# Kernel optimization log

Measured on AMD Instinct MI355X. Metric: run time of the kernel, lower is better.

The kernel has to match this reference:

```python
import jax, jax.numpy as jnp
import numpy as np

HID = 3584
NH = 16
NKV = 8
HD = 256
T = 2048
THETA = 10000.0
SCALE = 256.0 ** -0.5          # query_pre_attn_scalar ** -0.5
SOFT_CAP = 50.0                # Gemma2 attn_logits_soft_cap


def setup_inputs() -> dict:
    key = jax.random.key(0)
    k1, k2, k3 = jax.random.split(key, 3)
    return {
        "positions": jnp.arange(T, dtype=jnp.int32),
        "hidden_states": jax.random.normal(k1, (T, HID), dtype=jnp.float32),
        "w_qkv": jax.random.normal(k2, (HID, (NH + 2 * NKV) * HD), dtype=jnp.float32) * 0.02,
        "w_o": jax.random.normal(k3, (NH * HD, HID), dtype=jnp.float32) * 0.02,
    }


def _apply_rope(x, positions):
    # neox-style rotary embedding over full head_dim
    d = x.shape[-1]
    inv_freq = 1.0 / (THETA ** (jnp.arange(0, d, 2, dtype=jnp.float32) / d))  # [d/2]
    freqs = positions.astype(jnp.float32)[:, None] * inv_freq[None, :]        # [T, d/2]
    cos = jnp.concatenate([jnp.cos(freqs)] * 2, axis=-1)[:, None, :]          # [T,1,d]
    sin = jnp.concatenate([jnp.sin(freqs)] * 2, axis=-1)[:, None, :]
    x1, x2 = jnp.split(x, 2, axis=-1)
    rotated = jnp.concatenate([-x2, x1], axis=-1)
    return x * cos + rotated * sin


def reference(positions, hidden_states, w_qkv, w_o):
    t = hidden_states.shape[0]
    qkv = hidden_states @ w_qkv                                   # [T, (NH+2*NKV)*HD]
    q = qkv[:, : NH * HD].reshape(t, NH, HD)
    k = qkv[:, NH * HD:(NH + NKV) * HD].reshape(t, NKV, HD)
    v = qkv[:, (NH + NKV) * HD:].reshape(t, NKV, HD)

    q = _apply_rope(q, positions)
    k = _apply_rope(k, positions)

    rep = NH // NKV                                               # GQA expansion
    k = jnp.repeat(k, rep, axis=1)                                # [T, NH, HD]
    v = jnp.repeat(v, rep, axis=1)

    scores = jnp.einsum("qhd,khd->hqk", q, k) * SCALE             # [NH, T, T]
    scores = SOFT_CAP * jnp.tanh(scores / SOFT_CAP)               # logit soft-cap
    causal = jnp.tril(jnp.ones((t, t), dtype=bool))
    scores = jnp.where(causal[None, :, :], scores, -jnp.inf)
    probs = jax.nn.softmax(scores, axis=-1)
    out = jnp.einsum("hqk,khd->qhd", probs, v).reshape(t, NH * HD)
    return out @ w_o                                              # [T, HID]
```

## Files before the change

kernel.cpp:

```cpp
#include <hip/hip_runtime.h>
#include <hip/hip_bf16.h>


#define T_SEQ 2048
#define HID_DIM 3584
#define NH 16
#define NKV 8
#define HD 256
#define QKV_N ((NH + 2 * NKV) * HD)
#define ATT_N (NH * HD)
#define V_OFF ((NH + NKV) * HD)

typedef __bf16 bf16_t;
typedef bf16_t bf16x8 __attribute__((ext_vector_type(8)));
typedef float f32x4 __attribute__((ext_vector_type(4)));

__device__ __forceinline__ void gload16(const bf16_t* g, bf16_t* l) {
  __builtin_amdgcn_global_load_lds(
      (const __attribute__((address_space(1))) unsigned int*)g,
      (__attribute__((address_space(3))) unsigned int*)l, 16, 0, 0);
}

__global__ __launch_bounds__(256) void convert_bf16(
    const float* __restrict__ in, bf16_t* __restrict__ out) {
  const long i = ((long)blockIdx.x * 256 + threadIdx.x) * 8;
  const float4 f0 = *(const float4*)(in + i);
  const float4 f1 = *(const float4*)(in + i + 4);
  bf16x8 v;
  v[0] = (bf16_t)f0.x; v[1] = (bf16_t)f0.y; v[2] = (bf16_t)f0.z; v[3] = (bf16_t)f0.w;
  v[4] = (bf16_t)f1.x; v[5] = (bf16_t)f1.y; v[6] = (bf16_t)f1.z; v[7] = (bf16_t)f1.w;
  *(bf16x8*)(out + i) = v;
}

__global__ __launch_bounds__(256) void transpose_bf16(
    const float* __restrict__ in, bf16_t* __restrict__ out, int K, int N) {
  __shared__ __align__(16) bf16_t tile[64][80];
  const int k0 = blockIdx.x * 64;
  const int n0 = blockIdx.y * 64;
  const int t = threadIdx.x;
  const int rr = t >> 4;
  const int rc = (t & 15) * 4;
#pragma unroll
  for (int i = 0; i < 4; ++i) {
    const int k = rr + i * 16;
    const float4 v = *(const float4*)(in + (long)(k0 + k) * N + n0 + rc);
    tile[rc + 0][k] = (bf16_t)v.x;
    tile[rc + 1][k] = (bf16_t)v.y;
    tile[rc + 2][k] = (bf16_t)v.z;
    tile[rc + 3][k] = (bf16_t)v.w;
  }
  __syncthreads();
  const int wn = t >> 3;
  const int wk = (t & 7) * 8;
#pragma unroll
  for (int i = 0; i < 2; ++i) {
    const int n = wn + i * 32;
    *(bf16x8*)(out + (long)(n0 + n) * K + k0 + wk) = *(const bf16x8*)&tile[n][wk];
  }
}

template <typename TC>
__global__ __launch_bounds__(256) void gemm_bt(
    const bf16_t* __restrict__ A, const bf16_t* __restrict__ Bt,
    TC* __restrict__ C, bf16_t* __restrict__ Vt, int voff,
    int M, int N, int K) {
  const int n0 = blockIdx.x * 128;
  const int m0 = blockIdx.y * 128;
  const int t = threadIdx.x;
  const int w = t >> 6;
  const int lane = t & 63;
  const int l16 = lane & 15;
  const int quad = lane >> 4;

  __shared__ __align__(16) bf16_t As[128][32];
  __shared__ __align__(16) bf16_t Bs[128][32];

  f32x4 acc[4][4];
#pragma unroll
  for (int i = 0; i < 4; ++i)
#pragma unroll
    for (int j = 0; j < 4; ++j) acc[i][j] = f32x4{0, 0, 0, 0};

  const int srow = lane >> 2;
  const int scol = (lane & 3) * 8;
  const bf16_t* gsrc;
  bf16_t* lbase;
  if (w < 2) {
    gsrc = A + (long)(m0 + w * 64 + srow) * K + scol;
    lbase = &As[w * 64][0];
  } else {
    gsrc = Bt + (long)(n0 + (w - 2) * 64 + srow) * K + scol;
    lbase = &Bs[(w - 2) * 64][0];
  }

  const int wm = w & 1;
  const int wn = w >> 1;

  for (int k0 = 0; k0 < K; k0 += 32) {
#pragma unroll
    for (int j = 0; j < 4; ++j)
      gload16(gsrc + (long)j * 16 * K + k0, lbase + j * (16 * 32));
    __syncthreads();

    bf16x8 af[4], bfr[4];
#pragma unroll
    for (int i = 0; i < 4; ++i) {
      af[i] = *(const bf16x8*)&As[wm * 64 + i * 16 + l16][quad * 8];
      bfr[i] = *(const bf16x8*)&Bs[wn * 64 + i * 16 + l16][quad * 8];
    }
#pragma unroll
    for (int i = 0; i < 4; ++i)
#pragma unroll
      for (int j = 0; j < 4; ++j)
        acc[i][j] = __builtin_amdgcn_mfma_f32_16x16x32_bf16(af[i], bfr[j],
                                                            acc[i][j], 0, 0, 0);
    __syncthreads();
  }

#pragma unroll
  for (int i = 0; i < 4; ++i) {
    const int row = m0 + wm * 64 + i * 16 + quad * 4;
#pragma unroll
    for (int j = 0; j < 4; ++j) {
      const int col = n0 + wn * 64 + j * 16 + l16;
#pragma unroll
      for (int r = 0; r < 4; ++r) {
        if (col >= voff)
          Vt[(long)(col - voff) * QKV_N + (row + r)] = (bf16_t)acc[i][j][r];
        else
          C[(long)(row + r) * N + col] = (TC)acc[i][j][r];
      }
    }
  }
}

__global__ void rope_kernel(const int* __restrict__ positions,
                            bf16_t* __restrict__ qkv) {
  const int head = blockIdx.x;
  const int trow = blockIdx.y;
  const int d = threadIdx.x;
  const long col0 = (head < NH) ? (long)head * HD
                                : (long)(NH * HD) + (long)(head - NH) * HD;
  bf16_t* p = qkv + (long)trow * QKV_N + col0;
  const float pos = (float)positions[trow];
  const float inv_freq = exp2f(-(float)d * (13.287712379549449f / 128.0f));
  const float ang = pos * inv_freq;
  float s, c;
  sincosf(ang, &s, &c);
  const float x1 = (float)p[d];
  const float x2 = (float)p[d + 128];
  p[d]       = (bf16_t)(x1 * c - x2 * s);
  p[d + 128] = (bf16_t)(x2 * c + x1 * s);
}

__global__ __launch_bounds__(256) void attn_mfma(
    const bf16_t* __restrict__ qkv, const bf16_t* __restrict__ vt,
    bf16_t* __restrict__ out ) {
  const int lid = blockIdx.x;
  const int kvh = lid & 7;
  const int slot = lid >> 3;
  const int h = 2 * kvh + (slot & 1);
  const int ps = slot >> 1;
  const int pb = (ps < 16) ? ps : 47 - ps;
  const int t = threadIdx.x;
  const int w = t >> 6;
  const int lane = t & 63;
  const int l16 = lane & 15;
  const int quad = lane >> 4;
  const int chunk = (w < 2) ? (2 * pb + w) : (124 - 2 * pb + w);
  const int q0 = chunk * 16;
  const int ktiles = (chunk >> 1) + 1;

  __shared__ __align__(16) bf16_t Ps[4][16][40];

  bf16x8 qf[8];
  const bf16_t* qbase = qkv + (long)(q0 + l16) * QKV_N + h * HD + quad * 8;
#pragma unroll
  for (int s = 0; s < 8; ++s) qf[s] = *(const bf16x8*)(qbase + s * 32);

  const bf16_t* kbase = qkv + (long)l16 * QKV_N + (NH * HD) + kvh * HD + quad * 8;
  const bf16_t* vbase = vt + (long)(kvh * HD + l16) * QKV_N + quad * 8;

  f32x4 oacc[16];
#pragma unroll
  for (int nt = 0; nt < 16; ++nt) oacc[nt] = f32x4{0, 0, 0, 0};
  float m_state[4], l_state[4];
#pragma unroll
  for (int r = 0; r < 4; ++r) { m_state[r] = -1e30f; l_state[r] = 0.0f; }

  for (int kt = 0; kt < ktiles; ++kt) {
    bf16x8 kf[2][8];
    const bf16_t* kp = kbase + (long)(kt * 32) * QKV_N;
#pragma unroll
    for (int g = 0; g < 2; ++g)
#pragma unroll
      for (int s = 0; s < 8; ++s)
        kf[g][s] = *(const bf16x8*)(kp + (long)(g * 16) * QKV_N + s * 32);

    f32x4 sacc[2] = {f32x4{0, 0, 0, 0}, f32x4{0, 0, 0, 0}};
    __builtin_amdgcn_s_setprio(1);
#pragma unroll
    for (int g = 0; g < 2; ++g)
#pragma unroll
      for (int s = 0; s < 8; ++s)
        sacc[g] = __builtin_amdgcn_mfma_f32_16x16x32_bf16(qf[s], kf[g][s],
                                                          sacc[g], 0, 0, 0);
    __builtin_amdgcn_s_setprio(0);

    float alpha[4];
#pragma unroll
    for (int r = 0; r < 4; ++r) {
      const int row = q0 + quad * 4 + r;
      float svg[2];
      float best = -1e30f;
#pragma unroll
      for (int g = 0; g < 2; ++g) {
        const float x = sacc[g][r] * 0.0625f;
        const float e = __expf(x * 0.04f);
        const float tz = 50.0f * (e - 1.0f) / (e + 1.0f);
        const int col = kt * 32 + g * 16 + l16;
        svg[g] = (col <= row) ? tz : -1e30f;
        best = fmaxf(best, svg[g]);
      }
      best = fmaxf(best, __shfl_xor(best, 1));
      best = fmaxf(best, __shfl_xor(best, 2));
      best = fmaxf(best, __shfl_xor(best, 4));
      best = fmaxf(best, __shfl_xor(best, 8));
      const float mnew = fmaxf(m_state[r], best);
      float psum = 0.0f;
#pragma unroll
      for (int g = 0; g < 2; ++g) {
        const float pv = (svg[g] > -1e29f) ? __expf(svg[g] - mnew) : 0.0f;
        Ps[w][quad * 4 + r][g * 16 + l16] = (bf16_t)pv;
        psum += pv;
      }
      psum += __shfl_xor(psum, 1);
      psum += __shfl_xor(psum, 2);
      psum += __shfl_xor(psum, 4);
      psum += __shfl_xor(psum, 8);
      alpha[r] = __expf(m_state[r] - mnew);
      l_state[r] = l_state[r] * alpha[r] + psum;
      m_state[r] = mnew;
    }
#pragma unroll
    for (int nt = 0; nt < 16; ++nt) {
      oacc[nt][0] *= alpha[0];
      oacc[nt][1] *= alpha[1];
      oacc[nt][2] *= alpha[2];
      oacc[nt][3] *= alpha[3];
    }

    const bf16x8 pa = *(const bf16x8*)&Ps[w][l16][quad * 8];

#pragma unroll
    for (int h2 = 0; h2 < 2; ++h2) {
      bf16x8 vf[8];
#pragma unroll
      for (int nt = 0; nt < 8; ++nt)
        vf[nt] = *(const bf16x8*)(vbase + (long)(h2 * 128 + nt * 16) * QKV_N +
                                  kt * 32);
      __builtin_amdgcn_s_setprio(1);
#pragma unroll
      for (int nt = 0; nt < 8; ++nt)
        oacc[h2 * 8 + nt] = __builtin_amdgcn_mfma_f32_16x16x32_bf16(
            pa, vf[nt], oacc[h2 * 8 + nt], 0, 0, 0);
      __builtin_amdgcn_s_setprio(0);
    }
  }

#pragma unroll
  for (int r = 0; r < 4; ++r) {
    const float inv = 1.0f / l_state[r];
    bf16_t* op = out + (long)(q0 + quad * 4 + r) * ATT_N + h * HD + l16;
#pragma unroll
    for (int nt = 0; nt < 16; ++nt) op[nt * 16] = (bf16_t)(oacc[nt][r] * inv);
  }
}

extern "C" void kernel_launch(void* const* d_in, const int* in_sizes, int n_in,
                              void* d_out, int out_size, void* d_ws, size_t ws_size,
                              hipStream_t stream) {
  const int* positions = (const int*)d_in[0];
  const float* hidden = (const float*)d_in[1];
  const float* w_qkv = (const float*)d_in[2];
  const float* w_o = (const float*)d_in[3];
  float* out = (float*)d_out;

  bf16_t* qkv = (bf16_t*)d_ws;
  bf16_t* attn = qkv + (size_t)T_SEQ * QKV_N;
  bf16_t* hid_bf = attn + (size_t)T_SEQ * ATT_N;
  bf16_t* wqkv_t = hid_bf + (size_t)T_SEQ * HID_DIM;
  bf16_t* wo_t = wqkv_t + (size_t)QKV_N * HID_DIM;
  bf16_t* vtb = qkv + V_OFF;

  convert_bf16<<<(T_SEQ * HID_DIM) / 2048, 256, 0, stream>>>(hidden, hid_bf);
  transpose_bf16<<<dim3(HID_DIM / 64, QKV_N / 64), 256, 0, stream>>>(
      w_qkv, wqkv_t, HID_DIM, QKV_N);
  transpose_bf16<<<dim3(ATT_N / 64, HID_DIM / 64), 256, 0, stream>>>(
      w_o, wo_t, ATT_N, HID_DIM);

  gemm_bt<bf16_t><<<dim3(QKV_N / 128, T_SEQ / 128), 256, 0, stream>>>(
      hid_bf, wqkv_t, qkv, vtb, V_OFF, T_SEQ, QKV_N, HID_DIM);
  rope_kernel<<<dim3(NH + NKV, T_SEQ), 128, 0, stream>>>(positions, qkv);
  attn_mfma<<<512, 256, 0, stream>>>(qkv, vtb, attn);
  gemm_bt<float><<<dim3(HID_DIM / 128, T_SEQ / 128), 256, 0, stream>>>(
      attn, wo_t, out, attn , 1 << 30, T_SEQ, HID_DIM, ATT_N);
}
```

Baseline: 845.9 us.

## Prefetch K/V tiles ahead of use and skip softmax rescale unless max grows

The attention kernel now loads the next K tile into registers while the current tile's score MFMAs and softmax run. It also issues both V half-tiles before the softmax math so their latency overlaps. Softmax uses a lazy rescale: probabilities are computed against the old running max, and the oacc rescale and recompute only happen when some row's max exceeds the old one by more than 8. Smaller changes are a cheaper reciprocal in the tanh soft-cap and launch_bounds(256,2) for occupancy. The added live registers (two V fragment arrays plus prefetched K) may raise register pressure or cause spills.

```diff
diff --git a/kernel.cpp b/kernel.cpp
--- a/kernel.cpp
+++ b/kernel.cpp
@@ -153,15 +153,15 @@
   p[d + 128] = (bf16_t)(x2 * c + x1 * s);
 }
 
-__global__ __launch_bounds__(256) void attn_mfma(
+__global__ __launch_bounds__(256, 2) void attn_mfma(
     const bf16_t* __restrict__ qkv, const bf16_t* __restrict__ vt,
     bf16_t* __restrict__ out ) {
   const int lid = blockIdx.x;
   const int kvh = lid & 7;
   const int slot = lid >> 3;
   const int h = 2 * kvh + (slot & 1);
-  const int ps = slot >> 1;
-  const int pb = (ps < 16) ? ps : 47 - ps;
+  const int ps_ = slot >> 1;
+  const int pb = (ps_ < 16) ? ps_ : 47 - ps_;
   const int t = threadIdx.x;
   const int w = t >> 6;
   const int lane = t & 63;
@@ -188,84 +188,124 @@
 #pragma unroll
   for (int r = 0; r < 4; ++r) { m_state[r] = -1e30f; l_state[r] = 0.0f; }
 
+  bf16x8 kf[2][8];
+#pragma unroll
+  for (int g = 0; g < 2; ++g)
+#pragma unroll
+    for (int s = 0; s < 8; ++s)
+      kf[g][s] = *(const bf16x8*)(kbase + (long)(g * 16) * QKV_N + s * 32);
+
   for (int kt = 0; kt < ktiles; ++kt) {
-    bf16x8 kf[2][8];
-    const bf16_t* kp = kbase + (long)(kt * 32) * QKV_N;
-#pragma unroll
-    for (int g = 0; g < 2; ++g)
-#pragma unroll
-      for (int s = 0; s < 8; ++s)
-        kf[g][s] = *(const bf16x8*)(kp + (long)(g * 16) * QKV_N + s * 32);
-
     f32x4 sacc[2] = {f32x4{0, 0, 0, 0}, f32x4{0, 0, 0, 0}};
     __builtin_amdgcn_s_setprio(1);
 #pragma unroll
-    for (int g = 0; g < 2; ++g)
-#pragma unroll
-      for (int s = 0; s < 8; ++s)
+    for (int s = 0; s < 8; ++s)
+#pragma unroll
+      for (int g = 0; g < 2; ++g)
         sacc[g] = __builtin_amdgcn_mfma_f32_16x16x32_bf16(qf[s], kf[g][s],
                                                           sacc[g], 0, 0, 0);
     __builtin_amdgcn_s_setprio(0);
 
-    float alpha[4];
+    {
+      const int ktn = (kt + 1 < ktiles) ? (kt + 1) : kt;
+      const bf16_t* kp = kbase + (long)(ktn * 32) * QKV_N;
+#pragma unroll
+      for (int g = 0; g < 2; ++g)
+#pragma unroll
+        for (int s = 0; s < 8; ++s)
+          kf[g][s] = *(const bf16x8*)(kp + (long)(g * 16) * QKV_N + s * 32);
+    }
+
+    const bf16_t* vp = vbase + kt * 32;
+    bf16x8 vf0[8];
+#pragma unroll
+    for (int nt = 0; nt < 8; ++nt)
+      vf0[nt] = *(const bf16x8*)(vp + (long)(nt * 16) * QKV_N);
+
+    float sv[2][4], best[4], psl[4];
 #pragma unroll
     for (int r = 0; r < 4; ++r) {
       const int row = q0 + quad * 4 + r;
-      float svg[2];
-      float best = -1e30f;
+      const float m_old = m_state[r];
+      float b = -1e30f;
 #pragma unroll
       for (int g = 0; g < 2; ++g) {
         const float x = sacc[g][r] * 0.0625f;
         const float e = __expf(x * 0.04f);
-        const float tz = 50.0f * (e - 1.0f) / (e + 1.0f);
+        float tz = 50.0f * (e - 1.0f) * __builtin_amdgcn_rcpf(e + 1.0f);
         const int col = kt * 32 + g * 16 + l16;
-        svg[g] = (col <= row) ? tz : -1e30f;
-        best = fmaxf(best, svg[g]);
-      }
-      best = fmaxf(best, __shfl_xor(best, 1));
-      best = fmaxf(best, __shfl_xor(best, 2));
-      best = fmaxf(best, __shfl_xor(best, 4));
-      best = fmaxf(best, __shfl_xor(best, 8));
-      const float mnew = fmaxf(m_state[r], best);
-      float psum = 0.0f;
-#pragma unroll
-      for (int g = 0; g < 2; ++g) {
-        const float pv = (svg[g] > -1e29f) ? __expf(svg[g] - mnew) : 0.0f;
-        Ps[w][quad * 4 + r][g * 16 + l16] = (bf16_t)pv;
-        psum += pv;
-      }
-      psum += __shfl_xor(psum, 1);
-      psum += __shfl_xor(psum, 2);
-      psum += __shfl_xor(psum, 4);
-      psum += __shfl_xor(psum, 8);
-      alpha[r] = __expf(m_state[r] - mnew);
-      l_state[r] = l_state[r] * alpha[r] + psum;
-      m_state[r] = mnew;
-    }
-#pragma unroll
-    for (int nt = 0; nt < 16; ++nt) {
-      oacc[nt][0] *= alpha[0];
-      oacc[nt][1] *= alpha[1];
-      oacc[nt][2] *= alpha[2];
-      oacc[nt][3] *= alpha[3];
+        tz = (col <= row) ? tz : -1e30f;
+        sv[g][r] = tz;
+        b = fmaxf(b, tz);
+      }
+      best[r] = b;
+      const float p0 = __expf(sv[0][r] - m_old);
+      const float p1 = __expf(sv[1][r] - m_old);
+      Ps[w][quad * 4 + r][l16] = (bf16_t)p0;
+      Ps[w][quad * 4 + r][16 + l16] = (bf16_t)p1;
+      psl[r] = p0 + p1;
+    }
+
+    bf16x8 vf1[8];
+#pragma unroll
+    for (int nt = 0; nt < 8; ++nt)
+      vf1[nt] = *(const bf16x8*)(vp + (long)(128 + nt * 16) * QKV_N);
+
+#pragma unroll
+    for (int d = 1; d <= 8; d <<= 1) {
+#pragma unroll
+      for (int r = 0; r < 4; ++r) {
+        best[r] = fmaxf(best[r], __shfl_xor(best[r], d));
+        psl[r] += __shfl_xor(psl[r], d);
+      }
+    }
+
+    bool need = false;
+#pragma unroll
+    for (int r = 0; r < 4; ++r) need = need || (best[r] > m_state[r] + 8.0f);
+    if (__any(need)) {
+      float alpha[4];
+#pragma unroll
+      for (int r = 0; r < 4; ++r) {
+        const float m_old = m_state[r];
+        const float mnew = fmaxf(m_old, best[r]);
+        alpha[r] = __expf(m_old - mnew);
+        const float p0 = __expf(sv[0][r] - mnew);
+        const float p1 = __expf(sv[1][r] - mnew);
+        Ps[w][quad * 4 + r][l16] = (bf16_t)p0;
+        Ps[w][quad * 4 + r][16 + l16] = (bf16_t)p1;
+        float p01 = p0 + p1;
+        p01 += __shfl_xor(p01, 1);
+        p01 += __shfl_xor(p01, 2);
+        p01 += __shfl_xor(p01, 4);
+        p01 += __shfl_xor(p01, 8);
+        l_state[r] = l_state[r] * alpha[r] + p01;
+        m_state[r] = mnew;
+      }
+#pragma unroll
+      for (int nt = 0; nt < 16; ++nt) {
+        oacc[nt][0] *= alpha[0];
+        oacc[nt][1] *= alpha[1];
+        oacc[nt][2] *= alpha[2];
+        oacc[nt][3] *= alpha[3];
+      }
+    } else {
+#pragma unroll
+      for (int r = 0; r < 4; ++r) l_state[r] += psl[r];
     }
 
     const bf16x8 pa = *(const bf16x8*)&Ps[w][l16][quad * 8];
 
-#pragma unroll
-    for (int h2 = 0; h2 < 2; ++h2) {
-      bf16x8 vf[8];
-#pragma unroll
-      for (int nt = 0; nt < 8; ++nt)
-        vf[nt] = *(const bf16x8*)(vbase + (long)(h2 * 128 + nt * 16) * QKV_N +
-                                  kt * 32);
-      __builtin_amdgcn_s_setprio(1);
-#pragma unroll
-      for (int nt = 0; nt < 8; ++nt)
-        oacc[h2 * 8 + nt] = __builtin_amdgcn_mfma_f32_16x16x32_bf16(
-            pa, vf[nt], oacc[h2 * 8 + nt], 0, 0, 0);
-      __builtin_amdgcn_s_setprio(0);
-    }
+    __builtin_amdgcn_s_setprio(1);
+#pragma unroll
+    for (int nt = 0; nt < 8; ++nt)
+      oacc[nt] = __builtin_amdgcn_mfma_f32_16x16x32_bf16(pa, vf0[nt],
+                                                         oacc[nt], 0, 0, 0);
+#pragma unroll
+    for (int nt = 0; nt < 8; ++nt)
+      oacc[8 + nt] = __builtin_amdgcn_mfma_f32_16x16x32_bf16(pa, vf1[nt],
+                                                             oacc[8 + nt], 0, 0, 0);
+    __builtin_amdgcn_s_setprio(0);
   }
 
 #pragma unroll
```

Result: slower. 1.057 ms (+25.0%).

## Split attention KV range across warps with split-K softmax merge

Applied to the files above, without the earlier changes.

Each block now owns a single 16-row query chunk, and its four waves split that chunk's key tiles among themselves. The partial max, sum and output accumulators are then combined through shared memory using the log-sum-exp rescaling. Before, each wave handled its own query chunk, paired by causal length for balance. The grid grows from 512 to 2048 blocks, chunks are ordered longest-first, and launch bounds request 4 blocks per CU. The aim is more parallelism and better load balance, at the cost of extra LDS traffic, barriers and register pressure in the merge step.

```diff
diff --git a/kernel.cpp b/kernel.cpp
--- a/kernel.cpp
+++ b/kernel.cpp
@@ -153,25 +153,30 @@
   p[d + 128] = (bf16_t)(x2 * c + x1 * s);
 }
 
-__global__ __launch_bounds__(256) void attn_mfma(
+__global__ __launch_bounds__(256, 4) void attn_mfma(
     const bf16_t* __restrict__ qkv, const bf16_t* __restrict__ vt,
     bf16_t* __restrict__ out ) {
   const int lid = blockIdx.x;
   const int kvh = lid & 7;
   const int slot = lid >> 3;
   const int h = 2 * kvh + (slot & 1);
-  const int ps = slot >> 1;
-  const int pb = (ps < 16) ? ps : 47 - ps;
+  const int chunk = 127 - (slot >> 1);
+  const int q0 = chunk * 16;
+  const int ktiles = (chunk >> 1) + 1;
   const int t = threadIdx.x;
   const int w = t >> 6;
   const int lane = t & 63;
   const int l16 = lane & 15;
   const int quad = lane >> 4;
-  const int chunk = (w < 2) ? (2 * pb + w) : (124 - 2 * pb + w);
-  const int q0 = chunk * 16;
-  const int ktiles = (chunk >> 1) + 1;
+  const int base = ktiles >> 2;
+  const int rem = ktiles & 3;
+  const int cnt = base + (w < rem ? 1 : 0);
+  const int start = w * base + (w < rem ? w : rem);
 
   __shared__ __align__(16) bf16_t Ps[4][16][40];
+  __shared__ float sm[4][16], sl[4][16];
+  __shared__ __align__(16) float slabA[16][260];
+  __shared__ __align__(16) float slabB[16][260];
 
   bf16x8 qf[8];
   const bf16_t* qbase = qkv + (long)(q0 + l16) * QKV_N + h * HD + quad * 8;
@@ -188,7 +193,7 @@
 #pragma unroll
   for (int r = 0; r < 4; ++r) { m_state[r] = -1e30f; l_state[r] = 0.0f; }
 
-  for (int kt = 0; kt < ktiles; ++kt) {
+  for (int kt = start; kt < start + cnt; ++kt) {
     bf16x8 kf[2][8];
     const bf16_t* kp = kbase + (long)(kt * 32) * QKV_N;
 #pragma unroll
@@ -268,12 +273,76 @@
     }
   }
 
+  if (l16 == 0) {
+#pragma unroll
+    for (int r = 0; r < 4; ++r) {
+      sm[w][quad * 4 + r] = m_state[r];
+      sl[w][quad * 4 + r] = l_state[r];
+    }
+  }
+  __syncthreads();
+
+  float fac[4], lsum[4];
 #pragma unroll
   for (int r = 0; r < 4; ++r) {
-    const float inv = 1.0f / l_state[r];
-    bf16_t* op = out + (long)(q0 + quad * 4 + r) * ATT_N + h * HD + l16;
-#pragma unroll
-    for (int nt = 0; nt < 16; ++nt) op[nt * 16] = (bf16_t)(oacc[nt][r] * inv);
+    const int row = quad * 4 + r;
+    const float mstar = fmaxf(fmaxf(sm[0][row], sm[1][row]),
+                              fmaxf(sm[2][row], sm[3][row]));
+    fac[r] = __expf(m_state[r] - mstar);
+    float ls = 0.0f;
+#pragma unroll
+    for (int j = 0; j < 4; ++j) ls += __expf(sm[j][row] - mstar) * sl[j][row];
+    lsum[r] = ls;
+  }
+#pragma unroll
+  for (int nt = 0; nt < 16; ++nt) {
+    oacc[nt][0] *= fac[0];
+    oacc[nt][1] *= fac[1];
+    oacc[nt][2] *= fac[2];
+    oacc[nt][3] *= fac[3];
+  }
+
+  if (w == 1 || w == 3) {
+    float(*slab)[260] = (w == 1) ? slabA : slabB;
+#pragma unroll
+    for (int r = 0; r < 4; ++r)
+#pragma unroll
+      for (int nt = 0; nt < 16; ++nt)
+        slab[quad * 4 + r][nt * 16 + l16] = oacc[nt][r];
+  }
+  __syncthreads();
+  if (w == 0) {
+#pragma unroll
+    for (int r = 0; r < 4; ++r)
+#pragma unroll
+      for (int nt = 0; nt < 16; ++nt)
+        oacc[nt][r] += slabA[quad * 4 + r][nt * 16 + l16];
+  } else if (w == 2) {
+#pragma unroll
+    for (int r = 0; r < 4; ++r)
+#pragma unroll
+      for (int nt = 0; nt < 16; ++nt)
+        oacc[nt][r] += slabB[quad * 4 + r][nt * 16 + l16];
+  }
+  __syncthreads();
+  if (w == 2) {
+#pragma unroll
+    for (int r = 0; r < 4; ++r)
+#pragma unroll
+      for (int nt = 0; nt < 16; ++nt)
+        slabA[quad * 4 + r][nt * 16 + l16] = oacc[nt][r];
+  }
+  __syncthreads();
+  if (w == 0) {
+#pragma unroll
+    for (int r = 0; r < 4; ++r) {
+      const float inv = 1.0f / lsum[r];
+      bf16_t* op = out + (long)(q0 + quad * 4 + r) * ATT_N + h * HD + l16;
+#pragma unroll
+      for (int nt = 0; nt < 16; ++nt)
+        op[nt * 16] =
+            (bf16_t)((oacc[nt][r] + slabA[quad * 4 + r][nt * 16 + l16]) * inv);
+    }
   }
 }
 
@@ -302,7 +371,7 @@
   gemm_bt<bf16_t><<<dim3(QKV_N / 128, T_SEQ / 128), 256, 0, stream>>>(
       hid_bf, wqkv_t, qkv, vtb, V_OFF, T_SEQ, QKV_N, HID_DIM);
   rope_kernel<<<dim3(NH + NKV, T_SEQ), 128, 0, stream>>>(positions, qkv);
-  attn_mfma<<<512, 256, 0, stream>>>(qkv, vtb, attn);
+  attn_mfma<<<2048, 256, 0, stream>>>(qkv, vtb, attn);
   gemm_bt<float><<<dim3(HID_DIM / 128, T_SEQ / 128), 256, 0, stream>>>(
       attn, wo_t, out, attn , 1 << 30, T_SEQ, HID_DIM, ATT_N);
 }
```

After: 1.076 ms. 1.27x slower.

## Share K/V tiles in LDS across waves and drop online softmax max tracking

Applied to the files above, without the earlier changes.

The attention kernel now assigns a block of four waves to 64 consecutive query rows of one head. K and V tiles are staged into double-buffered, swizzled LDS with async global-to-LDS loads, so all waves share each fetch and the next tile's load overlaps current compute. Because the soft-capped logits are bounded by 50, the running max and rescaling are removed: probabilities are computed directly as exp(capped - 50) via exp2/rcp, and the row sums are accumulated with an MFMA against a ones vector. The costs are heavy-first ordering without the previous pairing-based load balance, a barrier per tile, and reliance on fixed cap bounds for numerical safety.

```diff
diff --git a/kernel.cpp b/kernel.cpp
--- a/kernel.cpp
+++ b/kernel.cpp
@@ -158,120 +158,121 @@
     bf16_t* __restrict__ out ) {
   const int lid = blockIdx.x;
   const int kvh = lid & 7;
-  const int slot = lid >> 3;
-  const int h = 2 * kvh + (slot & 1);
-  const int ps = slot >> 1;
-  const int pb = (ps < 16) ? ps : 47 - ps;
+  const int h = 2 * kvh + ((lid >> 3) & 1);
+  const int slot = lid >> 4;
+  const int chunk = 31 - slot;
+  const int q0 = chunk * 64;
+  const int ktiles = 2 * chunk + 2;
   const int t = threadIdx.x;
   const int w = t >> 6;
   const int lane = t & 63;
   const int l16 = lane & 15;
   const int quad = lane >> 4;
-  const int chunk = (w < 2) ? (2 * pb + w) : (124 - 2 * pb + w);
-  const int q0 = chunk * 16;
-  const int ktiles = (chunk >> 1) + 1;
-
+
+  __shared__ __align__(16) bf16_t Ks[2][32 * 256];
+  __shared__ __align__(16) bf16_t Vs[2][256 * 32];
   __shared__ __align__(16) bf16_t Ps[4][16][40];
 
+  const float C1 = 0.0036067376022224085f;
+  const float C2 = -144.26950408889634f;
+
   bf16x8 qf[8];
-  const bf16_t* qbase = qkv + (long)(q0 + l16) * QKV_N + h * HD + quad * 8;
+  const bf16_t* qbase =
+      qkv + (long)(q0 + w * 16 + l16) * QKV_N + h * HD + quad * 8;
 #pragma unroll
   for (int s = 0; s < 8; ++s) qf[s] = *(const bf16x8*)(qbase + s * 32);
 
-  const bf16_t* kbase = qkv + (long)l16 * QKV_N + (NH * HD) + kvh * HD + quad * 8;
-  const bf16_t* vbase = vt + (long)(kvh * HD + l16) * QKV_N + quad * 8;
+  bf16x8 onesf;
+#pragma unroll
+  for (int j = 0; j < 8; ++j) onesf[j] = (bf16_t)1.0f;
 
   f32x4 oacc[16];
 #pragma unroll
   for (int nt = 0; nt < 16; ++nt) oacc[nt] = f32x4{0, 0, 0, 0};
-  float m_state[4], l_state[4];
-#pragma unroll
-  for (int r = 0; r < 4; ++r) { m_state[r] = -1e30f; l_state[r] = 0.0f; }
-
+  f32x4 lacc = f32x4{0, 0, 0, 0};
+
+  const bf16_t* kglob = qkv + (long)(NH * HD) + kvh * HD;
+  const bf16_t* vglob = vt + (long)(kvh * HD) * QKV_N;
+
+  auto STAGE = [&](int kt_, int b) {
+#pragma unroll
+    for (int j = 0; j < 4; ++j) {
+      const int U = j * 256 + w * 64 + lane;
+      const int row = U >> 5, u = U & 31;
+      gload16(kglob + (long)(kt_ * 32 + row) * QKV_N + ((u ^ (row & 7)) << 3),
+              &Ks[b][(j * 256 + w * 64) * 8]);
+    }
+#pragma unroll
+    for (int j = 0; j < 4; ++j) {
+      const int U = j * 256 + w * 64 + lane;
+      const int row = U >> 2, u = U & 3;
+      gload16(vglob + (long)row * QKV_N + kt_ * 32 + ((u ^ (row & 3)) << 3),
+              &Vs[b][(j * 256 + w * 64) * 8]);
+    }
+  };
+
+  STAGE(0, 0);
+  __syncthreads();
+
+  int cur = 0;
   for (int kt = 0; kt < ktiles; ++kt) {
-    bf16x8 kf[2][8];
-    const bf16_t* kp = kbase + (long)(kt * 32) * QKV_N;
-#pragma unroll
-    for (int g = 0; g < 2; ++g)
-#pragma unroll
-      for (int s = 0; s < 8; ++s)
-        kf[g][s] = *(const bf16x8*)(kp + (long)(g * 16) * QKV_N + s * 32);
+    if (kt + 1 < ktiles) STAGE(kt + 1, cur ^ 1);
 
     f32x4 sacc[2] = {f32x4{0, 0, 0, 0}, f32x4{0, 0, 0, 0}};
     __builtin_amdgcn_s_setprio(1);
 #pragma unroll
-    for (int g = 0; g < 2; ++g)
-#pragma unroll
-      for (int s = 0; s < 8; ++s)
-        sacc[g] = __builtin_amdgcn_mfma_f32_16x16x32_bf16(qf[s], kf[g][s],
+    for (int g = 0; g < 2; ++g) {
+      const int krow = g * 16 + l16;
+      const bf16_t* kr = &Ks[cur][krow * 256];
+      const int sw = l16 & 7;
+#pragma unroll
+      for (int s = 0; s < 8; ++s) {
+        const bf16x8 kf = *(const bf16x8*)(kr + (((quad + s * 4) ^ sw) << 3));
+        sacc[g] = __builtin_amdgcn_mfma_f32_16x16x32_bf16(qf[s], kf,
                                                           sacc[g], 0, 0, 0);
+      }
+    }
     __builtin_amdgcn_s_setprio(0);
 
-    float alpha[4];
 #pragma unroll
     for (int r = 0; r < 4; ++r) {
-      const int row = q0 + quad * 4 + r;
-      float svg[2];
-      float best = -1e30f;
+      const int row = q0 + w * 16 + quad * 4 + r;
 #pragma unroll
       for (int g = 0; g < 2; ++g) {
-        const float x = sacc[g][r] * 0.0625f;
-        const float e = __expf(x * 0.04f);
-        const float tz = 50.0f * (e - 1.0f) / (e + 1.0f);
+        const float e2 = exp2f(sacc[g][r] * C1);
+        float p = exp2f(C2 * __builtin_amdgcn_rcpf(e2 + 1.0f));
         const int col = kt * 32 + g * 16 + l16;
-        svg[g] = (col <= row) ? tz : -1e30f;
-        best = fmaxf(best, svg[g]);
+        p = (col <= row) ? p : 0.0f;
+        Ps[w][quad * 4 + r][g * 16 + l16] = (bf16_t)p;
       }
-      best = fmaxf(best, __shfl_xor(best, 1));
-      best = fmaxf(best, __shfl_xor(best, 2));
-      best = fmaxf(best, __shfl_xor(best, 4));
-      best = fmaxf(best, __shfl_xor(best, 8));
-      const float mnew = fmaxf(m_state[r], best);
-      float psum = 0.0f;
-#pragma unroll
-      for (int g = 0; g < 2; ++g) {
-        const float pv = (svg[g] > -1e29f) ? __expf(svg[g] - mnew) : 0.0f;
-        Ps[w][quad * 4 + r][g * 16 + l16] = (bf16_t)pv;
-        psum += pv;
+    }
+
+    const bf16x8 pa = *(const bf16x8*)&Ps[w][l16][quad * 8];
+
+    __builtin_amdgcn_s_setprio(1);
+    lacc = __builtin_amdgcn_mfma_f32_16x16x32_bf16(pa, onesf, lacc, 0, 0, 0);
+    {
+      const int sw = l16 & 3;
+#pragma unroll
+      for (int nt = 0; nt < 16; ++nt) {
+        const bf16x8 vf =
+            *(const bf16x8*)(&Vs[cur][(nt * 16 + l16) * 32] +
+                             ((quad ^ sw) << 3));
+        oacc[nt] = __builtin_amdgcn_mfma_f32_16x16x32_bf16(pa, vf,
+                                                           oacc[nt], 0, 0, 0);
       }
-      psum += __shfl_xor(psum, 1);
-      psum += __shfl_xor(psum, 2);
-      psum += __shfl_xor(psum, 4);
-      psum += __shfl_xor(psum, 8);
-      alpha[r] = __expf(m_state[r] - mnew);
-      l_state[r] = l_state[r] * alpha[r] + psum;
-      m_state[r] = mnew;
-    }
-#pragma unroll
-    for (int nt = 0; nt < 16; ++nt) {
-      oacc[nt][0] *= alpha[0];
-      oacc[nt][1] *= alpha[1];
-      oacc[nt][2] *= alpha[2];
-      oacc[nt][3] *= alpha[3];
-    }
-
-    const bf16x8 pa = *(const bf16x8*)&Ps[w][l16][quad * 8];
-
-#pragma unroll
-    for (int h2 = 0; h2 < 2; ++h2) {
-      bf16x8 vf[8];
-#pragma unroll
-      for (int nt = 0; nt < 8; ++nt)
-        vf[nt] = *(const bf16x8*)(vbase + (long)(h2 * 128 + nt * 16) * QKV_N +
-                                  kt * 32);
-      __builtin_amdgcn_s_setprio(1);
-#pragma unroll
-      for (int nt = 0; nt < 8; ++nt)
-        oacc[h2 * 8 + nt] = __builtin_amdgcn_mfma_f32_16x16x32_bf16(
-            pa, vf[nt], oacc[h2 * 8 + nt], 0, 0, 0);
-      __builtin_amdgcn_s_setprio(0);
-    }
+    }
+    __builtin_amdgcn_s_setprio(0);
+
+    __syncthreads();
+    cur ^= 1;
   }
 
 #pragma unroll
   for (int r = 0; r < 4; ++r) {
-    const float inv = 1.0f / l_state[r];
-    bf16_t* op = out + (long)(q0 + quad * 4 + r) * ATT_N + h * HD + l16;
+    const float inv = 1.0f / lacc[r];
+    bf16_t* op =
+        out + (long)(q0 + w * 16 + quad * 4 + r) * ATT_N + h * HD + l16;
 #pragma unroll
     for (int nt = 0; nt < 16; ++nt) op[nt * 16] = (bf16_t)(oacc[nt][r] * inv);
   }
```

Result: faster. 691.3 us (-18.3%).
